# Optimization experiments

Hardware: AMD Instinct MI355X
Metric: run time of the kernel (lower is better)

## Reference

```python
import jax, jax.numpy as jnp
import numpy as np

NEAR_THRESHOLD = 0.25
N = 1536          # entities (== max_entities)
D = 768           # d_model
H = 64            # classifier hidden width
NTYPES = 4        # relation types: 0=NEAR, 1=APPROACHING, 2=FLEEING, 3=ABOVE
SPATIAL = 8       # geometric feature dim


def setup_inputs() -> dict:
    key = jax.random.key(0)
    ks = jax.random.split(key, 6)
    entity_embeddings = jax.random.normal(ks[0], (N, D), dtype=jnp.float32)
    positions = jax.random.uniform(ks[1], (N, 3), dtype=jnp.float32)
    prev_positions = jax.random.uniform(ks[2], (N, 3), dtype=jnp.float32)
    in_dim = 2 * D + SPATIAL
    W1 = jax.random.normal(ks[3], (in_dim, H), dtype=jnp.float32) * (1.0 / np.sqrt(in_dim))
    b1 = jnp.zeros((H,), dtype=jnp.float32)
    W2 = jax.random.normal(ks[4], (H, NTYPES), dtype=jnp.float32) * (1.0 / np.sqrt(H))
    b2 = jnp.zeros((NTYPES,), dtype=jnp.float32)
    return {"entity_embeddings": entity_embeddings, "positions": positions,
            "prev_positions": prev_positions, "W1": W1, "b1": b1, "W2": W2, "b2": b2}


def reference(entity_embeddings, positions, prev_positions, W1, b1, W2, b2):
    n, d = entity_embeddings.shape
    velocities = positions - prev_positions
    # pairwise geometry: entry [i, j] corresponds to pair (a=i, b=j)
    rel_pos = positions[None, :, :] - positions[:, None, :]      # (N, N, 3) = pos_b - pos_a
    rel_vel = velocities[None, :, :] - velocities[:, None, :]    # (N, N, 3)
    distance = jnp.linalg.norm(rel_pos, axis=-1)                 # (N, N)
    closing = -(rel_pos * rel_vel).sum(-1) / jnp.maximum(distance, 1e-6)
    vdiff = rel_pos[..., 1]
    # spatial feats = [dx, dy, dz, dist, dvx, dvy, dvz, vertical_diff]
    sp = jnp.concatenate([rel_pos, distance[..., None], rel_vel, vdiff[..., None]], axis=-1)  # (N, N, 8)

    # first Linear on concat([emb_a, emb_b, sp]) decomposed into three projections
    W1a, W1b, W1s = W1[:d], W1[d:2 * d], W1[2 * d:]
    ha = entity_embeddings @ W1a                                  # (N, H)
    hb = entity_embeddings @ W1b                                  # (N, H)
    hidden = jax.nn.relu(ha[:, None, :] + hb[None, :, :]
                         + jnp.einsum('ijs,sh->ijh', sp, W1s) + b1)  # (N, N, H)
    logits = hidden @ W2 + b2                                     # (N, N, 4)
    probs = jax.nn.softmax(logits, axis=-1)
    best_idx = jnp.argmax(probs, axis=-1)
    conf = jnp.max(probs, axis=-1)

    # conditional overrides (same priority order as _classify_pair)
    near = distance < NEAR_THRESHOLD
    appr = ~near & (closing > 0.05)
    flee = ~near & ~appr & (closing < -0.05)
    above = ~near & ~appr & ~flee & (jnp.abs(vdiff) > 0.3) & (distance < 0.5)
    rel_type = jnp.where(near, 0,
               jnp.where(appr, 1,
               jnp.where(flee, 2,
               jnp.where(above, 3, best_idx)))).astype(jnp.int32)
    conf_out = jnp.where(near, jnp.maximum(conf, 0.8),
               jnp.where(appr, jnp.maximum(conf, 0.6),
               jnp.where(flee, jnp.maximum(conf, 0.6),
               jnp.where(above, jnp.maximum(conf, 0.5), conf))))

    upper = jnp.triu(jnp.ones((n, n), dtype=bool), k=1)           # i < j pairs only
    valid = upper & (conf_out > 0.3)
    return rel_type, conf_out, valid
```

## Files before the change

### kernel.cpp

```cpp
#include <hip/hip_runtime.h>

typedef float f4 __attribute__((ext_vector_type(4)));
typedef float f2 __attribute__((ext_vector_type(2)));

#define N 1536
#define D 768
#define H 64
#define NN (N * N)

__global__ __launch_bounds__(256) void k1_gemm(
    const float* __restrict__ E, const float* __restrict__ pos,
    const float* __restrict__ ppos, const float* __restrict__ W1,
    const float* __restrict__ b1, float* __restrict__ P, int KC)
{
    __shared__ float Es[16][192];

    const int tid = threadIdx.x;
    const int i0  = blockIdx.x * 16;
    const int kcc = blockIdx.y;
    const int k0  = kcc * KC;

    const int hg  = tid & 31;
    const int h0  = hg * 4;
    const int mat = h0 >> 6;
    const int hc  = h0 & 63;
    const int rp  = tid >> 5;
    const float* Wbase = W1 + (size_t)(mat * D + k0) * H + hc;

    f4 acc0 = {0.f, 0.f, 0.f, 0.f};
    f4 acc1 = {0.f, 0.f, 0.f, 0.f};

    for (int ks = 0; ks < KC; ks += 192) {
        if (ks) __syncthreads();
        for (int f = tid; f < 16 * 48; f += 256) {
            int row = f / 48, c = f - row * 48;
            *(f4*)&Es[row][c * 4] =
                *(const f4*)&E[(size_t)(i0 + row) * D + k0 + ks + c * 4];
        }
        __syncthreads();

        const float* Wc  = Wbase + (size_t)ks * H;
        const float* e0p = Es[2 * rp];
        const float* e1p = Es[2 * rp + 1];
        for (int kk = 0; kk < 192; kk += 8) {
#pragma unroll
            for (int u = 0; u < 8; ++u) {
                f4 w = *(const f4*)&Wc[(size_t)(kk + u) * H];
                float e0 = e0p[kk + u], e1 = e1p[kk + u];
                acc0 = __builtin_elementwise_fma((f4){e0, e0, e0, e0}, w, acc0);
                acc1 = __builtin_elementwise_fma((f4){e1, e1, e1, e1}, w, acc1);
            }
        }
    }

    if (kcc == 0) {
        const float* Ws = W1 + (size_t)2 * D * H + hc;
        f4 wp0 = *(const f4*)&Ws[0 * H];
        f4 wp1 = *(const f4*)&Ws[1 * H] + *(const f4*)&Ws[7 * H];
        f4 wp2 = *(const f4*)&Ws[2 * H];
        f4 wv0 = *(const f4*)&Ws[4 * H];
        f4 wv1 = *(const f4*)&Ws[5 * H];
        f4 wv2 = *(const f4*)&Ws[6 * H];
        f4 bb  = *(const f4*)&b1[hc];
#pragma unroll
        for (int r = 0; r < 2; ++r) {
            int i = i0 + 2 * rp + r;
            float px = pos[3 * i], py = pos[3 * i + 1], pz = pos[3 * i + 2];
            float vx = px - ppos[3 * i];
            float vy = py - ppos[3 * i + 1];
            float vz = pz - ppos[3 * i + 2];
            f4 g = px * wp0 + py * wp1 + pz * wp2 + vx * wv0 + vy * wv1 + vz * wv2;
            f4 add = (mat == 0) ? (bb - g) : g;
            if (r == 0) acc0 += add; else acc1 += add;
        }
    }

#pragma unroll
    for (int r = 0; r < 2; ++r) {
        int i = i0 + 2 * rp + r;
        f4 a = r ? acc1 : acc0;
#pragma unroll
        for (int c = 0; c < 4; ++c)
            P[(size_t)(kcc * 128 + h0 + c) * N + i] = a[c];
    }
}

__global__ __launch_bounds__(256) void k2_main(
    const float* __restrict__ P, int nkc,
    const float* __restrict__ W1, const float* __restrict__ W2,
    const float* __restrict__ b2, const float* __restrict__ pos,
    const float* __restrict__ ppos, float* __restrict__ out)
{
    __shared__ float As[64][32];
    __shared__ f4 Bs[64][16];
    __shared__ float w3s[64];
    __shared__ f4 W2s[64];
    __shared__ float pis[32][3], vis[32][3], pjs[64][3], vjs[64][3];

    const int tid = threadIdx.x;
    const int i0 = blockIdx.y * 32;
    const int j0 = blockIdx.x * 64;

#pragma unroll
    for (int g = 0; g < 2; ++g) {
        int f = g * 256 + tid;
        int h = f >> 3, c = f & 7;
        f4 s = {0.f, 0.f, 0.f, 0.f};
        for (int kc = 0; kc < nkc; ++kc)
            s += *(const f4*)&P[(size_t)(kc * 128 + h) * N + i0 + c * 4];
        *(f4*)&As[h][c * 4] = s;
    }
#pragma unroll
    for (int g = 0; g < 4; ++g) {
        int f = g * 256 + tid;
        int h = f >> 4, c = f & 15;
        f4 s = {0.f, 0.f, 0.f, 0.f};
        for (int kc = 0; kc < nkc; ++kc)
            s += *(const f4*)&P[(size_t)(kc * 128 + 64 + h) * N + j0 + c * 4];
        Bs[h][c] = s;
    }
    if (tid < 64) {
        w3s[tid] = W1[(size_t)(2 * D + 3) * H + tid];
        W2s[tid] = *(const f4*)&W2[tid * 4];
        int j = j0 + tid;
        float px = pos[3 * j], py = pos[3 * j + 1], pz = pos[3 * j + 2];
        pjs[tid][0] = px; pjs[tid][1] = py; pjs[tid][2] = pz;
        vjs[tid][0] = px - ppos[3 * j];
        vjs[tid][1] = py - ppos[3 * j + 1];
        vjs[tid][2] = pz - ppos[3 * j + 2];
    } else if (tid < 96) {
        int t = tid - 64;
        int i = i0 + t;
        float px = pos[3 * i], py = pos[3 * i + 1], pz = pos[3 * i + 2];
        pis[t][0] = px; pis[t][1] = py; pis[t][2] = pz;
        vis[t][0] = px - ppos[3 * i];
        vis[t][1] = py - ppos[3 * i + 1];
        vis[t][2] = pz - ppos[3 * i + 2];
    }
    __syncthreads();

    const int tx = tid & 15;
    const int ty = tid >> 4;

    float dist[2][4];
    {
#pragma clang fp contract(off)
#pragma unroll
        for (int a = 0; a < 2; ++a) {
#pragma unroll
            for (int b = 0; b < 4; ++b) {
                int il = ty * 2 + a, jl = tx * 4 + b;
                float dx = pjs[jl][0] - pis[il][0];
                float dy = pjs[jl][1] - pis[il][1];
                float dz = pjs[jl][2] - pis[il][2];
                float s = dx * dx;
                s = s + dy * dy;
                s = s + dz * dz;
                dist[a][b] = sqrtf(s);
            }
        }
    }

    f2 d2[2][2];
#pragma unroll
    for (int a = 0; a < 2; ++a)
#pragma unroll
        for (int p = 0; p < 2; ++p)
            d2[a][p] = (f2){dist[a][2 * p], dist[a][2 * p + 1]};

    f2 acc[2][2][4];
#pragma unroll
    for (int a = 0; a < 2; ++a)
#pragma unroll
        for (int p = 0; p < 2; ++p)
#pragma unroll
            for (int l = 0; l < 4; ++l)
                acc[a][p][l] = (f2){0.f, 0.f};

#pragma unroll 8
    for (int h = 0; h < 64; ++h) {
        f2 Ai = *(const f2*)&As[h][ty * 2];
        f4 B4 = Bs[h][tx];
        float w3h = w3s[h];
        f4 w2r = W2s[h];
        f2 w3v = (f2){w3h, w3h};
        f2 wl0 = (f2){w2r.x, w2r.x};
        f2 wl1 = (f2){w2r.y, w2r.y};
        f2 wl2 = (f2){w2r.z, w2r.z};
        f2 wl3 = (f2){w2r.w, w2r.w};
#pragma unroll
        for (int a = 0; a < 2; ++a) {
            f2 Aa = (f2){Ai[a], Ai[a]};
#pragma unroll
            for (int p = 0; p < 2; ++p) {
                f2 Bp = (f2){B4[2 * p], B4[2 * p + 1]};
                f2 pre = Aa + Bp;
                f2 hid = __builtin_elementwise_fma(d2[a][p], w3v, pre);
                hid = __builtin_elementwise_max(hid, (f2){0.f, 0.f});
                acc[a][p][0] = __builtin_elementwise_fma(hid, wl0, acc[a][p][0]);
                acc[a][p][1] = __builtin_elementwise_fma(hid, wl1, acc[a][p][1]);
                acc[a][p][2] = __builtin_elementwise_fma(hid, wl2, acc[a][p][2]);
                acc[a][p][3] = __builtin_elementwise_fma(hid, wl3, acc[a][p][3]);
            }
        }
    }

    const f4 B2v = *(const f4*)b2;

#pragma unroll
    for (int a = 0; a < 2; ++a) {
        int il = ty * 2 + a;
        int i = i0 + il;
        f4 rt4, cf4, vl4;
#pragma unroll
        for (int b = 0; b < 4; ++b) {
            int jl = tx * 4 + b;
            int j = j0 + jl;
            int p = b >> 1, ln = b & 1;
            float dd = dist[a][b];
            float dy, closing;
            {
#pragma clang fp contract(off)
                float dx = pjs[jl][0] - pis[il][0];
                dy       = pjs[jl][1] - pis[il][1];
                float dz = pjs[jl][2] - pis[il][2];
                float rvx = vjs[jl][0] - vis[il][0];
                float rvy = vjs[jl][1] - vis[il][1];
                float rvz = vjs[jl][2] - vis[il][2];
                float dot = dx * rvx;
                dot = dot + dy * rvy;
                dot = dot + dz * rvz;
                closing = -dot / fmaxf(dd, 1e-6f);
            }
            float l0 = acc[a][p][0][ln] + B2v.x;
            float l1 = acc[a][p][1][ln] + B2v.y;
            float l2 = acc[a][p][2][ln] + B2v.z;
            float l3 = acc[a][p][3][ln] + B2v.w;
            float mx = l0; int bidx = 0;
            if (l1 > mx) { mx = l1; bidx = 1; }
            if (l2 > mx) { mx = l2; bidx = 2; }
            if (l3 > mx) { mx = l3; bidx = 3; }
            float s = expf(l0 - mx);
            s += expf(l1 - mx);
            s += expf(l2 - mx);
            s += expf(l3 - mx);
            float conf = 1.0f / s;

            bool near = dd < 0.25f;
            bool appr = !near && (closing > 0.05f);
            bool flee = !near && !appr && (closing < -0.05f);
            bool above = !near && !appr && !flee && (fabsf(dy) > 0.3f) && (dd < 0.5f);
            int rt = near ? 0 : appr ? 1 : flee ? 2 : above ? 3 : bidx;
            float co = near  ? fmaxf(conf, 0.8f)
                     : appr  ? fmaxf(conf, 0.6f)
                     : flee  ? fmaxf(conf, 0.6f)
                     : above ? fmaxf(conf, 0.5f)
                             : conf;
            float vd = ((j > i) && (co > 0.3f)) ? 1.0f : 0.0f;
            rt4[b] = (float)rt;
            cf4[b] = co;
            vl4[b] = vd;
        }
        int col = j0 + tx * 4;
        *(f4*)&out[(size_t)i * N + col]                  = rt4;
        *(f4*)&out[(size_t)NN + (size_t)i * N + col]     = cf4;
        *(f4*)&out[(size_t)2 * NN + (size_t)i * N + col] = vl4;
    }
}

extern "C" void kernel_launch(void* const* d_in, const int* in_sizes, int n_in,
                              void* d_out, int out_size, void* d_ws, size_t ws_size,
                              hipStream_t stream)
{
    const float* E    = (const float*)d_in[0];
    const float* pos  = (const float*)d_in[1];
    const float* ppos = (const float*)d_in[2];
    const float* W1   = (const float*)d_in[3];
    const float* b1   = (const float*)d_in[4];
    const float* W2   = (const float*)d_in[5];
    const float* b2   = (const float*)d_in[6];
    float* out = (float*)d_out;
    float* P   = (float*)d_ws;

    int nkc = (ws_size >= (size_t)4 * 128 * N * 4) ? 4 : 1;
    int KC  = D / nkc;

    dim3 g1(N / 16, nkc);
    k1_gemm<<<g1, 256, 0, stream>>>(E, pos, ppos, W1, b1, P, KC);

    dim3 g2(N / 64, N / 32);
    k2_main<<<g2, 256, 0, stream>>>(P, nkc, W1, W2, b2, pos, ppos, out);
}
```

Measured before the change: 130.2 us.

## Enlarge per-thread pair tile to 4x4 and halve block size in both kernels

The main kernel now uses 128 threads per block, each computing a 4x4 tile of pairs instead of 2x4. The inner hidden-unit loop is restructured so each hidden value is computed as a scalar and broadcast into an f4 FMA against the W2 row, instead of using paired f2 vectors. The goal is more register reuse of the A/B hidden projections and fewer shared-memory loads per pair. The GEMM kernel is also shrunk to 8-row blocks of 128 threads. Per-thread register use rises (16 f4 accumulators), which may lower occupancy, and the smaller blocks of the main kernel cut per-block parallelism.

```diff
diff --git a/kernel.cpp b/kernel.cpp
--- a/kernel.cpp
+++ b/kernel.cpp
@@ -1,22 +1,21 @@
 #include <hip/hip_runtime.h>
 
 typedef float f4 __attribute__((ext_vector_type(4)));
-typedef float f2 __attribute__((ext_vector_type(2)));
 
 #define N 1536
 #define D 768
 #define H 64
 #define NN (N * N)
 
-__global__ __launch_bounds__(256) void k1_gemm(
+__global__ __launch_bounds__(128) void k1_gemm(
     const float* __restrict__ E, const float* __restrict__ pos,
     const float* __restrict__ ppos, const float* __restrict__ W1,
     const float* __restrict__ b1, float* __restrict__ P, int KC)
 {
-    __shared__ float Es[16][192];
+    __shared__ float Es[8][192];
 
     const int tid = threadIdx.x;
-    const int i0  = blockIdx.x * 16;
+    const int i0  = blockIdx.x * 8;
     const int kcc = blockIdx.y;
     const int k0  = kcc * KC;
 
@@ -32,7 +31,7 @@
 
     for (int ks = 0; ks < KC; ks += 192) {
         if (ks) __syncthreads();
-        for (int f = tid; f < 16 * 48; f += 256) {
+        for (int f = tid; f < 8 * 48; f += 128) {
             int row = f / 48, c = f - row * 48;
             *(f4*)&Es[row][c * 4] =
                 *(const f4*)&E[(size_t)(i0 + row) * D + k0 + ks + c * 4];
@@ -85,7 +84,7 @@
     }
 }
 
-__global__ __launch_bounds__(256) void k2_main(
+__global__ __launch_bounds__(128) void k2_main(
     const float* __restrict__ P, int nkc,
     const float* __restrict__ W1, const float* __restrict__ W2,
     const float* __restrict__ b2, const float* __restrict__ pos,
@@ -102,8 +101,8 @@
     const int j0 = blockIdx.x * 64;
 
 #pragma unroll
-    for (int g = 0; g < 2; ++g) {
-        int f = g * 256 + tid;
+    for (int g = 0; g < 4; ++g) {
+        int f = g * 128 + tid;
         int h = f >> 3, c = f & 7;
         f4 s = {0.f, 0.f, 0.f, 0.f};
         for (int kc = 0; kc < nkc; ++kc)
@@ -111,8 +110,8 @@
         *(f4*)&As[h][c * 4] = s;
     }
 #pragma unroll
-    for (int g = 0; g < 4; ++g) {
-        int f = g * 256 + tid;
+    for (int g = 0; g < 8; ++g) {
+        int f = g * 128 + tid;
         int h = f >> 4, c = f & 15;
         f4 s = {0.f, 0.f, 0.f, 0.f};
         for (int kc = 0; kc < nkc; ++kc)
@@ -142,14 +141,14 @@
     const int tx = tid & 15;
     const int ty = tid >> 4;
 
-    float dist[2][4];
+    float dist[4][4];
     {
 #pragma clang fp contract(off)
 #pragma unroll
-        for (int a = 0; a < 2; ++a) {
+        for (int a = 0; a < 4; ++a) {
 #pragma unroll
             for (int b = 0; b < 4; ++b) {
-                int il = ty * 2 + a, jl = tx * 4 + b;
+                int il = ty * 4 + a, jl = tx * 4 + b;
                 float dx = pjs[jl][0] - pis[il][0];
                 float dy = pjs[jl][1] - pis[il][1];
                 float dz = pjs[jl][2] - pis[il][2];
@@ -161,46 +160,27 @@
         }
     }
 
-    f2 d2[2][2];
-#pragma unroll
-    for (int a = 0; a < 2; ++a)
-#pragma unroll
-        for (int p = 0; p < 2; ++p)
-            d2[a][p] = (f2){dist[a][2 * p], dist[a][2 * p + 1]};
-
-    f2 acc[2][2][4];
-#pragma unroll
-    for (int a = 0; a < 2; ++a)
-#pragma unroll
-        for (int p = 0; p < 2; ++p)
-#pragma unroll
-            for (int l = 0; l < 4; ++l)
-                acc[a][p][l] = (f2){0.f, 0.f};
-
-#pragma unroll 8
+    f4 acc[4][4];
+#pragma unroll
+    for (int a = 0; a < 4; ++a)
+#pragma unroll
+        for (int b = 0; b < 4; ++b)
+            acc[a][b] = (f4){0.f, 0.f, 0.f, 0.f};
+
+#pragma unroll 4
     for (int h = 0; h < 64; ++h) {
-        f2 Ai = *(const f2*)&As[h][ty * 2];
+        f4 A4 = *(const f4*)&As[h][ty * 4];
         f4 B4 = Bs[h][tx];
         float w3h = w3s[h];
         f4 w2r = W2s[h];
-        f2 w3v = (f2){w3h, w3h};
-        f2 wl0 = (f2){w2r.x, w2r.x};
-        f2 wl1 = (f2){w2r.y, w2r.y};
-        f2 wl2 = (f2){w2r.z, w2r.z};
-        f2 wl3 = (f2){w2r.w, w2r.w};
-#pragma unroll
-        for (int a = 0; a < 2; ++a) {
-            f2 Aa = (f2){Ai[a], Ai[a]};
-#pragma unroll
-            for (int p = 0; p < 2; ++p) {
-                f2 Bp = (f2){B4[2 * p], B4[2 * p + 1]};
-                f2 pre = Aa + Bp;
-                f2 hid = __builtin_elementwise_fma(d2[a][p], w3v, pre);
-                hid = __builtin_elementwise_max(hid, (f2){0.f, 0.f});
-                acc[a][p][0] = __builtin_elementwise_fma(hid, wl0, acc[a][p][0]);
-                acc[a][p][1] = __builtin_elementwise_fma(hid, wl1, acc[a][p][1]);
-                acc[a][p][2] = __builtin_elementwise_fma(hid, wl2, acc[a][p][2]);
-                acc[a][p][3] = __builtin_elementwise_fma(hid, wl3, acc[a][p][3]);
+#pragma unroll
+        for (int a = 0; a < 4; ++a) {
+#pragma unroll
+            for (int b = 0; b < 4; ++b) {
+                float hid = fmaf(dist[a][b], w3h, A4[a] + B4[b]);
+                hid = fmaxf(hid, 0.f);
+                acc[a][b] = __builtin_elementwise_fma(
+                    (f4){hid, hid, hid, hid}, w2r, acc[a][b]);
             }
         }
     }
@@ -208,15 +188,14 @@
     const f4 B2v = *(const f4*)b2;
 
 #pragma unroll
-    for (int a = 0; a < 2; ++a) {
-        int il = ty * 2 + a;
+    for (int a = 0; a < 4; ++a) {
+        int il = ty * 4 + a;
         int i = i0 + il;
         f4 rt4, cf4, vl4;
 #pragma unroll
         for (int b = 0; b < 4; ++b) {
             int jl = tx * 4 + b;
             int j = j0 + jl;
-            int p = b >> 1, ln = b & 1;
             float dd = dist[a][b];
             float dy, closing;
             {
@@ -232,18 +211,15 @@
                 dot = dot + dz * rvz;
                 closing = -dot / fmaxf(dd, 1e-6f);
             }
-            float l0 = acc[a][p][0][ln] + B2v.x;
-            float l1 = acc[a][p][1][ln] + B2v.y;
-            float l2 = acc[a][p][2][ln] + B2v.z;
-            float l3 = acc[a][p][3][ln] + B2v.w;
-            float mx = l0; int bidx = 0;
-            if (l1 > mx) { mx = l1; bidx = 1; }
-            if (l2 > mx) { mx = l2; bidx = 2; }
-            if (l3 > mx) { mx = l3; bidx = 3; }
-            float s = expf(l0 - mx);
-            s += expf(l1 - mx);
-            s += expf(l2 - mx);
-            s += expf(l3 - mx);
+            f4 l = acc[a][b] + B2v;
+            float mx = l.x; int bidx = 0;
+            if (l.y > mx) { mx = l.y; bidx = 1; }
+            if (l.z > mx) { mx = l.z; bidx = 2; }
+            if (l.w > mx) { mx = l.w; bidx = 3; }
+            float s = expf(l.x - mx);
+            s += expf(l.y - mx);
+            s += expf(l.z - mx);
+            s += expf(l.w - mx);
             float conf = 1.0f / s;
 
             bool near = dd < 0.25f;
@@ -285,9 +261,9 @@
     int nkc = (ws_size >= (size_t)4 * 128 * N * 4) ? 4 : 1;
     int KC  = D / nkc;
 
-    dim3 g1(N / 16, nkc);
-    k1_gemm<<<g1, 256, 0, stream>>>(E, pos, ppos, W1, b1, P, KC);
+    dim3 g1(N / 8, nkc);
+    k1_gemm<<<g1, 128, 0, stream>>>(E, pos, ppos, W1, b1, P, KC);
 
     dim3 g2(N / 64, N / 32);
-    k2_main<<<g2, 256, 0, stream>>>(P, nkc, W1, W2, b2, pos, ppos, out);
+    k2_main<<<g2, 128, 0, stream>>>(P, nkc, W1, W2, b2, pos, ppos, out);
 }
```

Result: slower. 150.3 us (+15.5%).
